# Optimization experiments

Measured on AMD Instinct MI355X. Metric: run time of the kernel, lower is better.

The kernel has to match this reference:

```python
import jax, jax.numpy as jnp
import numpy as np

B, SEQ, K, H = 4096, 50, 4, 64   # batch, seq_len, interest_num, hidden_size
ROUTING_TIMES = 3


def setup_inputs() -> dict:
    key = jax.random.key(0)
    k1, k2, k3 = jax.random.split(key, 3)
    mask = jax.random.randint(k1, (B, SEQ), 0, 2, dtype=jnp.int32)
    item_eb_hat = jax.random.normal(k2, (B, SEQ, K, H), dtype=jnp.float32)
    capsule_weight = jax.random.normal(k3, (B, K, SEQ), dtype=jnp.float32)
    return {"mask": mask, "item_eb_hat": item_eb_hat, "capsule_weight": capsule_weight}


def _squash(v):
    # v: [B, K, 1, H]
    cap_norm = jnp.sum(jnp.square(v), -1, keepdims=True)
    scalar = cap_norm / (1.0 + cap_norm) / jnp.sqrt(cap_norm + 1e-9)
    return scalar * v


def reference(mask, item_eb_hat, capsule_weight):
    # [B, seq, K, H] -> [B, K, seq, H]
    x = jnp.transpose(item_eb_hat.reshape(-1, SEQ, K, H), (0, 2, 1, 3))
    x_iter = jax.lax.stop_gradient(x)  # stop_grad=True in the module
    # attention mask broadcast to [B, K, seq]
    am = jnp.broadcast_to(mask[:, None, :], capsule_weight.shape)
    interest_capsule = None
    for i in range(ROUTING_TIMES):
        # torch F.softmax without dim on a 3D tensor -> dim=0 (batch axis); faithful.
        w = jax.nn.softmax(capsule_weight, axis=0)
        w = jnp.where(am == 0, jnp.zeros_like(w), w)[:, :, None, :]  # [B,K,1,seq]
        if i < ROUTING_TIMES - 1:
            interest_capsule = _squash(jnp.matmul(w, x_iter))          # [B,K,1,H]
            delta = jnp.matmul(x_iter, jnp.swapaxes(interest_capsule, -1, -2))  # [B,K,seq,1]
            capsule_weight = capsule_weight + delta.reshape(-1, K, SEQ)
        else:
            interest_capsule = _squash(jnp.matmul(w, x))               # [B,K,1,H]
    return interest_capsule.reshape(-1, K, H)
```

## Files before the change

### kernel.cpp

```cpp
#include <hip/hip_runtime.h>
#include <math.h>

#define BB 4096
#define SEQ 50
#define KK 4
#define HH 64
#define NCOL (KK*SEQ)
#define NPART 64
#define BPP (BB/NPART)

__device__ __forceinline__ float readlane_f32(float v, int lane) {
    return __int_as_float(__builtin_amdgcn_readlane(__float_as_int(v), lane));
}

__global__ void init_kernel(const float* __restrict__ cw,
                            float* __restrict__ part0,
                            float* __restrict__ part1,
                            float* __restrict__ part2) {
    const int p = blockIdx.x;
    const int t = threadIdx.x;
    if (t < NCOL) {
        const float* row = cw + (size_t)p * BPP * NCOL + t;
        float s = 0.f;
#pragma unroll 8
        for (int b = 0; b < BPP; b++) s += __expf(row[b * NCOL]);
        part0[p * NCOL + t] = s;
        part1[p * NCOL + t] = 0.f;
        part2[p * NCOL + t] = 0.f;
    }
}

template <int ITER>
__global__ __launch_bounds__(256, 4)
void update_kernel(const float* __restrict__ cw_src,
                   float* __restrict__ cw_dst,
                   const float* __restrict__ x,
                   const int* __restrict__ mask,
                   const float* __restrict__ part_in,
                   float* __restrict__ part_out,
                   float* __restrict__ out) {
    const int b = blockIdx.x;
    const int k = threadIdx.x >> 6;
    const int h = threadIdx.x & 63;

    __shared__ float scol[NCOL];

    if (threadIdx.x < NCOL) {
        float s = 0.f;
#pragma unroll 16
        for (int p = 0; p < NPART; p++) s += part_in[p * NCOL + threadIdx.x];
        scol[threadIdx.x] = s;
    }
    __syncthreads();

    float wlane = 0.f, c = 0.f;
    if (h < SEQ) {
        c = cw_src[(size_t)b * NCOL + k * SEQ + h];
        float e = __expf(c) / scol[k * SEQ + h];
        wlane = (mask[b * SEQ + h] != 0) ? e : 0.f;
    }

    const float* xp = x + (size_t)b * (SEQ * KK * HH) + k * HH + h;
    float v = 0.f;
#pragma unroll
    for (int s = 0; s < SEQ; s++)
        v = fmaf(readlane_f32(wlane, s), xp[s * (KK * HH)], v);

    float n2 = v * v;
#pragma unroll
    for (int off = 32; off >= 1; off >>= 1) n2 += __shfl_xor(n2, off, 64);
    const float scalar = n2 / ((1.f + n2) * sqrtf(n2 + 1e-9f));
    v *= scalar;

    if (ITER == 2) {
        out[(size_t)b * (KK * HH) + k * HH + h] = v;
    } else {
        asm volatile("" ::: "memory");

        float cur[64];
#pragma unroll
        for (int s = 0; s < SEQ; s++) cur[s] = xp[s * (KK * HH)] * v;
#pragma unroll
        for (int s = SEQ; s < 64; s++) cur[s] = 0.f;

#pragma unroll
        for (int j = 0; j < 6; j++) {
            const int half = 32 >> j;
            const bool hi = (h >> j) & 1;
            float nxt[32];
#pragma unroll
            for (int i = 0; i < 32; i++) {
                if (i < half) {
                    float keep = hi ? cur[2 * i + 1] : cur[2 * i];
                    float send = hi ? cur[2 * i] : cur[2 * i + 1];
                    float recv = __shfl_xor(send, 1 << j, 64);
                    nxt[i] = keep + recv;
                }
            }
#pragma unroll
            for (int i = 0; i < 32; i++) {
                if (i < half) cur[i] = nxt[i];
            }
        }
        if (h < SEQ) {
            const float nc = c + cur[0];
            cw_dst[(size_t)b * NCOL + k * SEQ + h] = nc;
            atomicAdd(&part_out[(b >> 6) * NCOL + k * SEQ + h], __expf(nc));
        }
    }
}

extern "C" void kernel_launch(void* const* d_in, const int* in_sizes, int n_in,
                              void* d_out, int out_size, void* d_ws, size_t ws_size,
                              hipStream_t stream) {
    const int*   mask  = (const int*)d_in[0];
    const float* x     = (const float*)d_in[1];
    const float* cw_in = (const float*)d_in[2];
    float* out = (float*)d_out;

    float* cw_ws = (float*)d_ws;
    float* part0 = cw_ws + (size_t)BB * NCOL;
    float* part1 = part0 + NPART * NCOL;
    float* part2 = part1 + NPART * NCOL;

    init_kernel<<<NPART, 256, 0, stream>>>(cw_in, part0, part1, part2);
    update_kernel<0><<<BB, 256, 0, stream>>>(cw_in, cw_ws, x, mask, part0, part1, nullptr);
    update_kernel<1><<<BB, 256, 0, stream>>>(cw_ws, cw_ws, x, mask, part1, part2, nullptr);
    update_kernel<2><<<BB, 256, 0, stream>>>(cw_ws, nullptr, x, mask, part2, nullptr, out);
}
```

Baseline: 374.3 us.

## Compute routing delta via per-lane row dot products with broadcast capsule

Replaces the 64-register transpose-reduce butterfly, which computed the per-sequence delta with many cross-lane shuffles, with a per-lane dot product. Each lane reads its own x row as float4 loads and multiplies it by capsule values broadcast through readlane. This cuts shuffle traffic and register pressure, which is why occupancy is raised to 8 waves per SIMD through launch bounds. The cost is a second, uncoalesced strided read of x per lane, though the block has likely just touched that data and it may still be in cache.

```diff
diff --git a/kernel.cpp b/kernel.cpp
--- a/kernel.cpp
+++ b/kernel.cpp
@@ -31,7 +31,7 @@
 }
 
 template <int ITER>
-__global__ __launch_bounds__(256, 4)
+__global__ __launch_bounds__(256, 8)
 void update_kernel(const float* __restrict__ cw_src,
                    float* __restrict__ cw_dst,
                    const float* __restrict__ x,
@@ -72,38 +72,25 @@
     const float scalar = n2 / ((1.f + n2) * sqrtf(n2 + 1e-9f));
     v *= scalar;
 
+    asm volatile("" : "+v"(v));
+
     if (ITER == 2) {
         out[(size_t)b * (KK * HH) + k * HH + h] = v;
     } else {
-        asm volatile("" ::: "memory");
-
-        float cur[64];
-#pragma unroll
-        for (int s = 0; s < SEQ; s++) cur[s] = xp[s * (KK * HH)] * v;
-#pragma unroll
-        for (int s = SEQ; s < 64; s++) cur[s] = 0.f;
-
-#pragma unroll
-        for (int j = 0; j < 6; j++) {
-            const int half = 32 >> j;
-            const bool hi = (h >> j) & 1;
-            float nxt[32];
-#pragma unroll
-            for (int i = 0; i < 32; i++) {
-                if (i < half) {
-                    float keep = hi ? cur[2 * i + 1] : cur[2 * i];
-                    float send = hi ? cur[2 * i] : cur[2 * i + 1];
-                    float recv = __shfl_xor(send, 1 << j, 64);
-                    nxt[i] = keep + recv;
-                }
-            }
-#pragma unroll
-            for (int i = 0; i < 32; i++) {
-                if (i < half) cur[i] = nxt[i];
-            }
+        const int hs = (h < SEQ) ? h : (SEQ - 1);
+        const float4* xs = (const float4*)(x + (size_t)b * (SEQ * KK * HH)
+                                           + (size_t)hs * (KK * HH) + k * HH);
+        float d0 = 0.f, d1 = 0.f, d2 = 0.f, d3 = 0.f;
+#pragma unroll 4
+        for (int j = 0; j < HH / 4; j++) {
+            float4 xv = xs[j];
+            d0 = fmaf(xv.x, readlane_f32(v, 4 * j + 0), d0);
+            d1 = fmaf(xv.y, readlane_f32(v, 4 * j + 1), d1);
+            d2 = fmaf(xv.z, readlane_f32(v, 4 * j + 2), d2);
+            d3 = fmaf(xv.w, readlane_f32(v, 4 * j + 3), d3);
         }
         if (h < SEQ) {
-            const float nc = c + cur[0];
+            const float nc = c + ((d0 + d1) + (d2 + d3));
             cw_dst[(size_t)b * NCOL + k * SEQ + h] = nc;
             atomicAdd(&part_out[(b >> 6) * NCOL + k * SEQ + h], __expf(nc));
         }
```

New measurement: 389.5 us. 1.04x slower.
